# Optimization experiments

Measured on AMD Instinct MI355X. Metric: run time of the kernel, lower is better.

Reference implementation:

```python
import jax, jax.numpy as jnp
import numpy as np

B, D, H, N, K, C = 1024, 256, 512, 100000, 96, 10


def setup_inputs() -> dict:
    key = jax.random.key(0)
    ks = jax.random.split(key, 16)
    s = 0.02
    return {
        "x": jax.random.normal(ks[0], (B, D), jnp.float32),
        "candidate_x": jax.random.normal(ks[1], (N, D), jnp.float32),
        "candidate_labels": jax.random.randint(ks[2], (N,), 0, C, jnp.int32),
        "W_enc": jax.random.normal(ks[3], (D, H), jnp.float32) * s,
        "b_enc": jnp.zeros((H,), jnp.float32),
        "W_key": jax.random.normal(ks[4], (H, H), jnp.float32) * s,
        "b_key": jnp.zeros((H,), jnp.float32),
        "W_val": jax.random.normal(ks[5], (H, H), jnp.float32) * s,
        "b_val": jnp.zeros((H,), jnp.float32),
        "E_label": jax.random.normal(ks[6], (C, H), jnp.float32) * s,
        "W_t1": jax.random.normal(ks[7], (H, H), jnp.float32) * s,
        "b_t1": jnp.zeros((H,), jnp.float32),
        "W_t2": jax.random.normal(ks[8], (H, H), jnp.float32) * s,
    }


def reference(x, candidate_x, candidate_labels, W_enc, b_enc, W_key, b_key,
              W_val, b_val, E_label, W_t1, b_t1, W_t2):
    # Encode queries and candidates
    x_enc = x @ W_enc + b_enc                       # [B, H]
    cand_enc = candidate_x @ W_enc + b_enc          # [N, H]
    x_key = x_enc @ W_key + b_key                   # [B, H]
    cand_keys = cand_enc @ W_key + b_key            # [N, H]

    # Negative euclidean distance via GEMM expansion (compute-efficient cdist)
    q2 = jnp.sum(x_key * x_key, axis=-1, keepdims=True)        # [B, 1]
    c2 = jnp.sum(cand_keys * cand_keys, axis=-1)               # [N]
    d2 = q2 + c2[None, :] - 2.0 * (x_key @ cand_keys.T)        # [B, N]
    sim = -jnp.sqrt(jnp.maximum(d2, 0.0))                      # [B, N]

    # Top-k retrieval
    top_sims, top_idx = jax.lax.top_k(sim, K)                  # [B, K]

    cand_vals = cand_enc @ W_val + b_val                       # [N, H]
    label_emb = E_label[candidate_labels]                      # [N, H]

    ctx_keys = cand_keys[top_idx]                              # [B, K, H]
    ctx_labels = label_emb[top_idx]                            # [B, K, H]
    _ = cand_vals[top_idx]  # gathered values (unused by the original math)

    # Attention over retrieved context (softmax of top-k similarities)
    attn = jax.nn.softmax(top_sims, axis=1)                    # [B, K]

    # Correction MLP T (dropout is identity in eval mode)
    diff = x_key[:, None, :] - ctx_keys                        # [B, K, H]
    t_out = jax.nn.relu(diff @ W_t1 + b_t1) @ W_t2             # [B, K, H]

    ctx_vec = jnp.sum(attn[..., None] * (ctx_labels + t_out), axis=1)  # [B, H]
    return x_enc + ctx_vec
```

## Files before the change

### kernel.cpp

```cpp
#include <hip/hip_runtime.h>
#include <cfloat>
#include <cmath>

#define B_ 1024
#define D_ 256
#define H_ 512
#define N_ 100000
#define K_ 96
#define C_ 10
#define SAMP 4096
#define CAPC 4096
#define RCAP 15

typedef __attribute__((ext_vector_type(8))) short bf16x8;
typedef __attribute__((ext_vector_type(4))) float f32x4;

__device__ __forceinline__ float bf2f(ushort h) {
    union { unsigned u; float f; } v; v.u = ((unsigned)h) << 16; return v.f;
}
__device__ __forceinline__ ushort f2bf(float f) {
    union { float f; unsigned u; } v; v.f = f;
    unsigned u = v.u;
    unsigned r = (u + 0x7fffu + ((u >> 16) & 1u)) >> 16;
    return (ushort)r;
}
__device__ __forceinline__ unsigned f2key(float f) {
    unsigned u = __float_as_uint(f);
    return (u & 0x80000000u) ? ~u : (u | 0x80000000u);
}
__device__ __forceinline__ float d2_of(float acc, float q2, float c2) {
    return fmaxf(fmaf(-2.f, acc, q2 + c2), 0.f);
}

#define GLDS(g, l)                                                            \
    __builtin_amdgcn_global_load_lds(                                         \
        (const __attribute__((address_space(1))) void*)(g),                   \
        (__attribute__((address_space(3))) void*)(l), 16, 0, 0)

#define FENCE() asm volatile("" ::: "memory")

template <int RELU>
__global__ __launch_bounds__(256) void gemm_nn(const float* __restrict__ A,
                                               const float* __restrict__ Bm,
                                               const float* __restrict__ bias,
                                               float* __restrict__ Cm,
                                               int M, int N, int Kd) {
    __shared__ float sA[16][68];
    __shared__ float sB[16][64];
    const int t  = threadIdx.x;
    const int tx = t & 15, ty = t >> 4;
    const int m0 = blockIdx.y * 64;
    const int n0 = blockIdx.x * 64;
    const int lr = t >> 2;
    const int lk = (t & 3) << 2;
    const int bk = t >> 4;
    const int bn = (t & 15) << 2;

    float acc[4][4] = {};
    for (int k0 = 0; k0 < Kd; k0 += 16) {
        float4 av = make_float4(0.f, 0.f, 0.f, 0.f);
        if (m0 + lr < M)
            av = *(const float4*)(A + (size_t)(m0 + lr) * Kd + k0 + lk);
        sA[lk + 0][lr] = av.x; sA[lk + 1][lr] = av.y;
        sA[lk + 2][lr] = av.z; sA[lk + 3][lr] = av.w;
        float4 bv = *(const float4*)(Bm + (size_t)(k0 + bk) * N + n0 + bn);
        *(float4*)&sB[bk][bn] = bv;
        __syncthreads();
#pragma unroll
        for (int kk = 0; kk < 16; ++kk) {
            float4 a4 = *(const float4*)&sA[kk][ty << 2];
            float4 b4 = *(const float4*)&sB[kk][tx << 2];
            float ar[4] = {a4.x, a4.y, a4.z, a4.w};
            float br[4] = {b4.x, b4.y, b4.z, b4.w};
#pragma unroll
            for (int i = 0; i < 4; ++i)
#pragma unroll
                for (int j = 0; j < 4; ++j)
                    acc[i][j] = fmaf(ar[i], br[j], acc[i][j]);
        }
        __syncthreads();
    }
#pragma unroll
    for (int i = 0; i < 4; ++i) {
        int row = m0 + (ty << 2) + i;
        if (row < M) {
            int col = n0 + (tx << 2);
            float b0 = 0.f, b1 = 0.f, b2 = 0.f, b3 = 0.f;
            if (bias) { b0 = bias[col]; b1 = bias[col + 1]; b2 = bias[col + 2]; b3 = bias[col + 3]; }
            float4 o;
            o.x = acc[i][0] + b0; o.y = acc[i][1] + b1;
            o.z = acc[i][2] + b2; o.w = acc[i][3] + b3;
            if (RELU) {
                o.x = fmaxf(o.x, 0.f); o.y = fmaxf(o.y, 0.f);
                o.z = fmaxf(o.z, 0.f); o.w = fmaxf(o.w, 0.f);
            }
            *(float4*)(Cm + (size_t)row * N + col) = o;
        }
    }
}

template <int MODE, int SWZ>
__global__ __launch_bounds__(256) void gemm_nt(const ushort* __restrict__ A,
                                               const ushort* __restrict__ Bv,
                                               const float* __restrict__ bias,
                                               const float* __restrict__ q2v,
                                               const float* __restrict__ c2v,
                                               const float* __restrict__ thrv,
                                               float* __restrict__ candV,
                                               int* __restrict__ candI,
                                               int* __restrict__ cnt,
                                               void* __restrict__ Cout,
                                               int M, int Nlim, int K,
                                               int ldc, int nvalid, int per) {
    int m0, n0;
    if (SWZ == 0) {
        m0 = blockIdx.y * 128; n0 = blockIdx.x * 128;
    } else if (SWZ == 1) {
        int bid = blockIdx.x;
        int xcd = bid & 7, slot = bid >> 3;
        m0 = (slot & 7) * 128;
        n0 = (xcd * per + (slot >> 3)) * 128;
        if (n0 >= nvalid || m0 >= M) return;
    } else {
        int bid = blockIdx.x;
        int xcd = bid & 7, slot = bid >> 3;
        n0 = (slot & 3) * 128;
        m0 = (xcd * per + (slot >> 2)) * 128;
        if (m0 >= M) return;
    }

    __shared__ __align__(16) char smem[32768];
    const int t = threadIdx.x;
    const int lane = t & 63, w = t >> 6;
    const int wm = w & 1, wn = w >> 1;

    f32x4 acc[4][4];
#pragma unroll
    for (int i = 0; i < 4; ++i)
#pragma unroll
        for (int j = 0; j < 4; ++j)
            acc[i][j] = (f32x4){0.f, 0.f, 0.f, 0.f};

    const int la = lane & 15, lk = lane >> 4;
    const int aoff = (wm * 64 + la) * 64 + lk * 16;
    const int boff = (wn * 64 + la) * 64 + lk * 16;
    const int r_ = t >> 2, cc_ = (t & 3);

    auto stage = [&](int k0, int buf) {
#pragma unroll
        for (int q = 0; q < 2; ++q) {
            int r = r_ + q * 64;
            int ar = m0 + r; ar = (ar < M) ? ar : (M - 1);
            GLDS(A + (size_t)ar * K + k0 + cc_ * 8,
                 (char*)smem + buf * 8192 + (q * 256 + t) * 16);
            int br = n0 + r; br = (br < Nlim) ? br : (Nlim - 1);
            GLDS(Bv + (size_t)br * K + k0 + cc_ * 8,
                 (char*)smem + 16384 + buf * 8192 + (q * 256 + t) * 16);
        }
    };

    stage(0, 0);
    int cur = 0;
    for (int k0 = 0; k0 < K; k0 += 32) {
        if (k0 + 32 < K) {
            stage(k0 + 32, cur ^ 1);
            FENCE();
            asm volatile("s_waitcnt vmcnt(4)" ::: "memory");
        } else {
            FENCE();
            asm volatile("s_waitcnt vmcnt(0)" ::: "memory");
        }
        __builtin_amdgcn_s_barrier(); FENCE();

        bf16x8 af[4], bfr[4];
        const char* pA = (const char*)smem + cur * 8192 + aoff;
        const char* pB = (const char*)smem + 16384 + cur * 8192 + boff;
#pragma unroll
        for (int i = 0; i < 4; ++i)
            af[i] = *(const bf16x8*)(pA + i * 1024);
#pragma unroll
        for (int j = 0; j < 4; ++j)
            bfr[j] = *(const bf16x8*)(pB + j * 1024);
#pragma unroll
        for (int i = 0; i < 4; ++i)
#pragma unroll
            for (int j = 0; j < 4; ++j)
                acc[i][j] = __builtin_amdgcn_mfma_f32_16x16x32_bf16(
                    af[i], bfr[j], acc[i][j], 0, 0, 0);

        FENCE();
        asm volatile("s_waitcnt lgkmcnt(0)" ::: "memory");
        __builtin_amdgcn_s_barrier(); FENCE();
        cur ^= 1;
    }

    const int rl = (lane >> 4) * 4, cl = lane & 15;

    if (MODE == 5) {
        float* stV = (float*)smem;
        int*   stI = (int*)(smem + 7680);
        int*   stC = (int*)(smem + 15360);
        for (int r = t; r < 128; r += 256) stC[r] = 0;
        __syncthreads();
#pragma unroll
        for (int i = 0; i < 4; ++i) {
#pragma unroll
            for (int v = 0; v < 4; ++v) {
                int rloc = wm * 64 + i * 16 + rl + v;
                int gr = m0 + rloc;
                float q2b = q2v[gr];
                float th = thrv[gr];
#pragma unroll
                for (int j = 0; j < 4; ++j) {
                    int gc = n0 + wn * 64 + j * 16 + cl;
                    if (gc < nvalid) {
                        float d2 = d2_of(acc[i][j][v], q2b, c2v[gc]);
                        if (d2 <= th) {
                            int p = atomicAdd(&stC[rloc], 1);
                            if (p < RCAP) {
                                stV[rloc * RCAP + p] = d2;
                                stI[rloc * RCAP + p] = gc;
                            } else {
                                int gp = atomicAdd(&cnt[gr], 1);
                                if (gp < CAPC) {
                                    candV[(size_t)gr * CAPC + gp] = d2;
                                    candI[(size_t)gr * CAPC + gp] = gc;
                                }
                            }
                        }
                    }
                }
            }
        }
        __syncthreads();
        for (int r = t; r < 128; r += 256) {
            int n = stC[r]; if (n > RCAP) n = RCAP;
            if (n > 0) {
                int gr = m0 + r;
                int gb = atomicAdd(&cnt[gr], n);
                for (int q = 0; q < n; ++q) {
                    int pos = gb + q;
                    if (pos < CAPC) {
                        candV[(size_t)gr * CAPC + pos] = stV[r * RCAP + q];
                        candI[(size_t)gr * CAPC + pos] = stI[r * RCAP + q];
                    }
                }
            }
        }
        return;
    }

#pragma unroll
    for (int i = 0; i < 4; ++i) {
#pragma unroll
        for (int j = 0; j < 4; ++j) {
            int gc = n0 + wn * 64 + j * 16 + cl;
#pragma unroll
            for (int v = 0; v < 4; ++v) {
                int gr = m0 + wm * 64 + i * 16 + rl + v;
                if (gr < M && gc < nvalid) {
                    float val = acc[i][j][v];
                    if (MODE == 2) {
                        ((float*)Cout)[(size_t)gr * ldc + gc] = val;
                    } else if (MODE == 4) {
                        ((float*)Cout)[(size_t)gr * ldc + gc] = val + bias[gc];
                    } else {
                        if (MODE == 1 || MODE == 3) val += bias[gc];
                        if (MODE == 1) val = fmaxf(val, 0.f);
                        ((ushort*)Cout)[(size_t)gr * ldc + gc] = f2bf(val);
                    }
                }
            }
        }
    }
}

__global__ __launch_bounds__(256) void thr_select(const float* __restrict__ S,
                                                  int ld,
                                                  const float* __restrict__ q2v,
                                                  const float* __restrict__ c2v,
                                                  float* __restrict__ thrArr) {
    __shared__ unsigned keys[SAMP];
    __shared__ int hist[256];
    __shared__ int sel[2];
    const int b = blockIdx.x, t = threadIdx.x;
    const float q2b = q2v[b];
    for (int i = t; i < SAMP; i += 256)
        keys[i] = ~f2key(d2_of(S[(size_t)b * ld + i], q2b, c2v[i]));
    __syncthreads();
    unsigned prefix = 0, mask = 0;
    int rank = K_;
    for (int shift = 24; shift >= 0; shift -= 8) {
        hist[t & 255] = 0;
        __syncthreads();
        for (int i = t; i < SAMP; i += 256) {
            unsigned k = keys[i];
            if ((k & mask) == prefix) atomicAdd(&hist[(k >> shift) & 255], 1);
        }
        __syncthreads();
        if (t == 0) {
            int r = rank, d = 255;
            for (; d > 0; --d) { int c = hist[d]; if (r - c <= 0) break; r -= c; }
            sel[0] = d; sel[1] = (r < 1) ? 1 : r;
        }
        __syncthreads();
        prefix |= ((unsigned)sel[0]) << shift;
        rank = sel[1];
        mask |= (0xFFu << shift);
        __syncthreads();
    }
    if (t == 0) {
        unsigned key = ~prefix;
        thrArr[b] = __uint_as_float(key & 0x7FFFFFFFu);
    }
}

__global__ __launch_bounds__(256) void final_select(const float* __restrict__ candV,
                                                    const int* __restrict__ candI,
                                                    const int* __restrict__ cnt,
                                                    float* __restrict__ topV,
                                                    int* __restrict__ topI) {
    __shared__ unsigned keys[CAPC];
    __shared__ int hist[256];
    __shared__ int sel[2];
    __shared__ int poscnt, eqcnt;
    const int b = blockIdx.x, t = threadIdx.x;
    int n = cnt[b]; if (n > CAPC) n = CAPC;
    for (int i = t; i < n; i += 256)
        keys[i] = ~f2key(candV[(size_t)b * CAPC + i]);
    __syncthreads();
    unsigned prefix = 0, mask = 0;
    int rank = K_;
    for (int shift = 24; shift >= 0; shift -= 8) {
        hist[t & 255] = 0;
        __syncthreads();
        for (int i = t; i < n; i += 256) {
            unsigned k = keys[i];
            if ((k & mask) == prefix) atomicAdd(&hist[(k >> shift) & 255], 1);
        }
        __syncthreads();
        if (t == 0) {
            int r = rank, d = 255;
            for (; d > 0; --d) { int c = hist[d]; if (r - c <= 0) break; r -= c; }
            sel[0] = d; sel[1] = (r < 1) ? 1 : r;
        }
        __syncthreads();
        prefix |= ((unsigned)sel[0]) << shift;
        rank = sel[1];
        mask |= (0xFFu << shift);
        __syncthreads();
    }
    unsigned kth = prefix;
    if (t == 0) { poscnt = 0; eqcnt = 0; }
    __syncthreads();
    for (int i = t; i < n; i += 256) {
        if (keys[i] > kth) {
            int p = atomicAdd(&poscnt, 1);
            topV[b * K_ + p] = candV[(size_t)b * CAPC + i];
            topI[b * K_ + p] = candI[(size_t)b * CAPC + i];
        }
    }
    __syncthreads();
    int base = poscnt;
    for (int i = t; i < n; i += 256) {
        if (keys[i] == kth) {
            int p = atomicAdd(&eqcnt, 1);
            if (base + p < K_) {
                topV[b * K_ + base + p] = candV[(size_t)b * CAPC + i];
                topI[b * K_ + base + p] = candI[(size_t)b * CAPC + i];
            }
        }
    }
}

__global__ void init_cnt(int* cnt) {
    int i = blockIdx.x * 256 + threadIdx.x;
    if (i < B_) cnt[i] = 0;
}

__global__ void conv_f2b(const float* __restrict__ in, ushort* __restrict__ out, int n) {
    int i = (blockIdx.x * 256 + threadIdx.x) * 4;
    int stride = gridDim.x * 256 * 4;
    for (; i < n; i += stride) {
        float4 v = *(const float4*)(in + i);
        ushort4 o;
        o.x = f2bf(v.x); o.y = f2bf(v.y); o.z = f2bf(v.z); o.w = f2bf(v.w);
        *(ushort4*)(out + i) = o;
    }
}

__global__ __launch_bounds__(256) void transpose_f2b(const float* __restrict__ in,
                                                     ushort* __restrict__ out,
                                                     int R, int Cn) {
    __shared__ float tile[32][33];
    int bx = blockIdx.x * 32, by = blockIdx.y * 32;
    int tx = threadIdx.x & 31, ty = threadIdx.x >> 5;
    int x = bx + tx;
#pragma unroll
    for (int dy = 0; dy < 32; dy += 8) {
        int y = by + ty + dy;
        if (x < Cn && y < R) tile[ty + dy][tx] = in[(size_t)y * Cn + x];
    }
    __syncthreads();
    int ox = by + tx;
#pragma unroll
    for (int dy = 0; dy < 32; dy += 8) {
        int oy = bx + ty + dy;
        if (ox < R && oy < Cn) out[(size_t)oy * R + ox] = f2bf(tile[tx][ty + dy]);
    }
}

__global__ __launch_bounds__(64) void rowsq_b(const ushort* __restrict__ X,
                                              float* __restrict__ outv) {
    const int r = blockIdx.x, t = threadIdx.x;
    const ushort* p = X + (size_t)r * H_;
    ushort4 a = *(const ushort4*)(p + t * 4);
    ushort4 b = *(const ushort4*)(p + 256 + t * 4);
    float ax = bf2f(a.x), ay = bf2f(a.y), az = bf2f(a.z), aw = bf2f(a.w);
    float bx = bf2f(b.x), by = bf2f(b.y), bz = bf2f(b.z), bw = bf2f(b.w);
    float v = ax * ax + ay * ay + az * az + aw * aw +
              bx * bx + by * by + bz * bz + bw * bw;
    for (int off = 32; off > 0; off >>= 1) v += __shfl_down(v, off);
    if (t == 0) outv[r] = v;
}

__global__ __launch_bounds__(64) void q2x_k(const ushort* __restrict__ Xb,
                                            const float* __restrict__ Xf,
                                            const float* __restrict__ bc,
                                            float* __restrict__ outv) {
    const int r = blockIdx.x, t = threadIdx.x;
    const ushort* p  = Xb + (size_t)r * H_ + t * 8;
    const float*  xf = Xf + (size_t)r * H_ + t * 8;
    float nrm = 0.f, dot = 0.f;
#pragma unroll
    for (int j = 0; j < 8; ++j) {
        float v = bf2f(p[j]);
        nrm = fmaf(v, v, nrm);
        dot = fmaf(xf[j], bc[t * 8 + j], dot);
    }
    for (int off = 32; off > 0; off >>= 1) {
        nrm += __shfl_down(nrm, off);
        dot += __shfl_down(dot, off);
    }
    if (t == 0) outv[r] = nrm - 2.f * dot;
}

__global__ void bcomb_k(const float* __restrict__ b_enc,
                        const float* __restrict__ W_key,
                        const float* __restrict__ b_key,
                        float* __restrict__ b_comb) {
    int h = blockIdx.x * 256 + threadIdx.x;
    if (h >= H_) return;
    float acc = b_key[h];
    for (int m = 0; m < H_; ++m)
        acc = fmaf(b_enc[m], W_key[(size_t)m * H_ + h], acc);
    b_comb[h] = acc;
}

__global__ __launch_bounds__(128) void softmax_k(const float* __restrict__ topVal,
                                                 float* __restrict__ attn) {
    __shared__ float red[128];
    const int b = blockIdx.x, t = threadIdx.x;
    float v = (t < K_) ? -sqrtf(topVal[b * K_ + t]) : -FLT_MAX;
    red[t] = v; __syncthreads();
    for (int s = 64; s > 0; s >>= 1) {
        if (t < s) red[t] = fmaxf(red[t], red[t + s]);
        __syncthreads();
    }
    float m = red[0]; __syncthreads();
    float e = (t < K_) ? expf(v - m) : 0.f;
    red[t] = e; __syncthreads();
    for (int s = 64; s > 0; s >>= 1) {
        if (t < s) red[t] += red[t + s];
        __syncthreads();
    }
    float ssum = red[0];
    if (t < K_) attn[b * K_ + t] = e / ssum;
}

__global__ __launch_bounds__(256) void wsum_q(const float* __restrict__ attn,
                                              const int* __restrict__ topI,
                                              const float* __restrict__ P,
                                              const ushort* __restrict__ Q,
                                              ushort* __restrict__ hw) {
    __shared__ float aw[K_];
    __shared__ int ai[K_];
    const int b = blockIdx.x, t = threadIdx.x;
    if (t < K_) { aw[t] = attn[b * K_ + t]; ai[t] = topI[b * K_ + t]; }
    __syncthreads();
    const float p0 = P[(size_t)b * H_ + 2 * t];
    const float p1 = P[(size_t)b * H_ + 2 * t + 1];
    float a0 = 0.f, a1 = 0.f;
    for (int k = 0; k < K_; ++k) {
        float w = aw[k];
        ushort2 q = *(const ushort2*)(Q + (size_t)ai[k] * H_ + 2 * t);
        a0 = fmaf(w, fmaxf(p0 - bf2f(q.x), 0.f), a0);
        a1 = fmaf(w, fmaxf(p1 - bf2f(q.y), 0.f), a1);
    }
    ushort2 o; o.x = f2bf(a0); o.y = f2bf(a1);
    *(ushort2*)(hw + (size_t)b * H_ + 2 * t) = o;
}

__global__ __launch_bounds__(128) void gather_diff_b(const float* __restrict__ XK,
                                                     const ushort* __restrict__ CK,
                                                     const int* __restrict__ topI,
                                                     ushort* __restrict__ diff,
                                                     int b0) {
    const int r = blockIdx.x;
    const int b = b0 + r / K_;
    const int idx = topI[b * K_ + (r % K_)];
    const int t = threadIdx.x;
    float4 xv = *(const float4*)(XK + (size_t)b * H_ + t * 4);
    ushort4 cv = *(const ushort4*)(CK + (size_t)idx * H_ + t * 4);
    ushort4 o;
    o.x = f2bf(xv.x - bf2f(cv.x));
    o.y = f2bf(xv.y - bf2f(cv.y));
    o.z = f2bf(xv.z - bf2f(cv.z));
    o.w = f2bf(xv.w - bf2f(cv.w));
    *(ushort4*)(diff + (size_t)r * H_ + t * 4) = o;
}

__global__ __launch_bounds__(256) void wsum_h(const float* __restrict__ attn,
                                              const ushort* __restrict__ h,
                                              ushort* __restrict__ hw, int b0) {
    const int bl = blockIdx.x;
    const int b = b0 + bl;
    const int t = threadIdx.x;
    float a0 = 0.f, a1 = 0.f;
    const float* ap = attn + b * K_;
    for (int k = 0; k < K_; ++k) {
        float w = ap[k];
        const ushort* hr = h + (size_t)(bl * K_ + k) * H_;
        a0 = fmaf(w, bf2f(hr[t]), a0);
        a1 = fmaf(w, bf2f(hr[t + 256]), a1);
    }
    hw[(size_t)b * H_ + t]       = f2bf(a0);
    hw[(size_t)b * H_ + t + 256] = f2bf(a1);
}

__global__ __launch_bounds__(256) void final_out(const float* __restrict__ attn,
                                                 const int* __restrict__ topI,
                                                 const int* __restrict__ labels,
                                                 const float* __restrict__ E,
                                                 const float* __restrict__ tsum,
                                                 const float* __restrict__ xe,
                                                 float* __restrict__ out) {
    const int b = blockIdx.x, t = threadIdx.x;
    float a0 = 0.f, a1 = 0.f;
    for (int k = 0; k < K_; ++k) {
        float w = attn[b * K_ + k];
        int idx = topI[b * K_ + k];
        int lab = labels[idx];
        const float* el = E + (size_t)lab * H_;
        a0 = fmaf(w, el[t], a0);
        a1 = fmaf(w, el[t + 256], a1);
    }
    out[(size_t)b * H_ + t] =
        xe[(size_t)b * H_ + t] + a0 + tsum[(size_t)b * H_ + t];
    out[(size_t)b * H_ + t + 256] =
        xe[(size_t)b * H_ + t + 256] + a1 + tsum[(size_t)b * H_ + t + 256];
}

extern "C" void kernel_launch(void* const* d_in, const int* in_sizes, int n_in,
                              void* d_out, int out_size, void* d_ws, size_t ws_size,
                              hipStream_t stream) {
    const float* x      = (const float*)d_in[0];
    const float* cx     = (const float*)d_in[1];
    const int*   labels = (const int*)d_in[2];
    const float* W_enc  = (const float*)d_in[3];
    const float* b_enc  = (const float*)d_in[4];
    const float* W_key  = (const float*)d_in[5];
    const float* b_key  = (const float*)d_in[6];
    const float* E_label = (const float*)d_in[9];
    const float* W_t1   = (const float*)d_in[10];
    const float* b_t1   = (const float*)d_in[11];
    const float* W_t2   = (const float*)d_in[12];
    float* out = (float*)d_out;

    char* base = (char*)d_ws;
    size_t off = 0;
    auto take = [&](size_t n) -> char* {
        char* p = base + off;
        off = (off + n + 255) & ~(size_t)255;
        return p;
    };
    float*  Wc    = (float*)take((size_t)D_ * H_ * 4);
    float*  bc    = (float*)take((size_t)H_ * 4);
    ushort* WcT   = (ushort*)take((size_t)H_ * D_ * 2);
    ushort* Wcb   = (ushort*)take((size_t)D_ * H_ * 2);
    ushort* Wt1T  = (ushort*)take((size_t)H_ * H_ * 2);
    ushort* Wt2T  = (ushort*)take((size_t)H_ * H_ * 2);
    float*  xe    = (float*)take((size_t)B_ * H_ * 4);
    float*  xk    = (float*)take((size_t)B_ * H_ * 4);
    ushort* xkb   = (ushort*)take((size_t)B_ * H_ * 2);
    ushort* xprojb= (ushort*)take((size_t)B_ * D_ * 2);
    float*  q2x   = (float*)take((size_t)B_ * 4);
    ushort* ckb   = (ushort*)take((size_t)N_ * H_ * 2);
    float*  c2    = (float*)take((size_t)N_ * 4);
    float*  topV  = (float*)take((size_t)B_ * K_ * 4);
    int*    topI  = (int*)take((size_t)B_ * K_ * 4);
    float*  thr   = (float*)take((size_t)B_ * 4);
    float*  attn  = (float*)take((size_t)B_ * K_ * 4);
    int*    cnt   = (int*)take((size_t)B_ * 4);
    float*  candV = (float*)take((size_t)B_ * CAPC * 4);
    int*    candI = (int*)take((size_t)B_ * CAPC * 4);
    ushort* hwAll = (ushort*)take((size_t)B_ * H_ * 2);
    float*  tsum  = (float*)take((size_t)B_ * H_ * 4);
    float*  Pbuf  = (float*)take((size_t)B_ * H_ * 4);
    char*   big   = base + off;
    size_t rem = (ws_size > off) ? (ws_size - off) : 0;

    ushort* cxb = (ushort*)big;
    float* simSmall = (float*)candV;

    {
        dim3 g(H_ / 64, D_ / 64);
        gemm_nn<0><<<g, 256, 0, stream>>>(W_enc, W_key, nullptr, Wc, D_, H_, H_);
        bcomb_k<<<(H_ + 255) / 256, 256, 0, stream>>>(b_enc, W_key, b_key, bc);
        dim3 gt1((H_ + 31) / 32, (D_ + 31) / 32);
        transpose_f2b<<<gt1, 256, 0, stream>>>(Wc, WcT, D_, H_);
        conv_f2b<<<128, 256, 0, stream>>>(Wc, Wcb, D_ * H_);
        dim3 gt2((H_ + 31) / 32, (H_ + 31) / 32);
        transpose_f2b<<<gt2, 256, 0, stream>>>(W_t1, Wt1T, H_, H_);
        transpose_f2b<<<gt2, 256, 0, stream>>>(W_t2, Wt2T, H_, H_);
    }
    {
        dim3 gx(H_ / 64, B_ / 64);
        gemm_nn<0><<<gx, 256, 0, stream>>>(x, W_enc, b_enc, xe, B_, H_, D_);
        gemm_nn<0><<<gx, 256, 0, stream>>>(x, Wc, bc, xk, B_, H_, D_);
        conv_f2b<<<1024, 256, 0, stream>>>(xk, xkb, B_ * H_);
        conv_f2b<<<2048, 256, 0, stream>>>(cx, cxb, N_ * D_);
        dim3 gp(D_ / 128, B_ / 128);
        gemm_nt<0, 0><<<gp, 256, 0, stream>>>(
            xkb, Wcb, nullptr, nullptr, nullptr, nullptr, nullptr, nullptr,
            nullptr, xprojb, B_, D_, H_, D_, D_, 0);
        q2x_k<<<B_, 64, 0, stream>>>(xkb, xk, bc, q2x);
        dim3 gq(H_ / 128, B_ / 128);
        gemm_nt<4, 0><<<gq, 256, 0, stream>>>(
            xkb, Wt1T, b_t1, nullptr, nullptr, nullptr, nullptr, nullptr,
            nullptr, Pbuf, B_, H_, H_, H_, H_, 0);
    }
    {
        int mt = (N_ + 127) / 128;
        int mper = (mt + 7) / 8;
        gemm_nt<3, 2><<<8 * mper * 4, 256, 0, stream>>>(
            cxb, WcT, bc, nullptr, nullptr, nullptr, nullptr, nullptr, nullptr,
            ckb, N_, H_, D_, H_, H_, mper);
    }
    rowsq_b<<<N_, 64, 0, stream>>>(ckb, c2);

    {
        int nper = (SAMP / 128 + 7) / 8;
        gemm_nt<2, 1><<<64 * nper, 256, 0, stream>>>(
            xprojb, cxb, nullptr, nullptr, nullptr, nullptr, nullptr, nullptr,
            nullptr, simSmall, B_, N_, D_, SAMP, SAMP, nper);
        thr_select<<<B_, 256, 0, stream>>>(simSmall, SAMP, q2x, c2, thr);
    }
    init_cnt<<<(B_ + 255) / 256, 256, 0, stream>>>(cnt);
    {
        int NT = (N_ + 127) / 128;
        int nper = (NT + 7) / 8;
        gemm_nt<5, 1><<<64 * nper, 256, 0, stream>>>(
            xprojb, cxb, nullptr, q2x, c2, thr, candV, candI, cnt,
            nullptr, B_, N_, D_, 0, N_, nper);
    }
    final_select<<<B_, 256, 0, stream>>>(candV, candI, cnt, topV, topI);
    softmax_k<<<B_, 128, 0, stream>>>(topV, attn);

    if (rem >= (size_t)N_ * H_ * 2) {
        ushort* Qb = (ushort*)big;
        int mt = (N_ + 127) / 128;
        int mper = (mt + 7) / 8;
        gemm_nt<0, 2><<<8 * mper * 4, 256, 0, stream>>>(
            ckb, Wt1T, nullptr, nullptr, nullptr, nullptr, nullptr, nullptr,
            nullptr, Qb, N_, H_, H_, H_, H_, mper);
        wsum_q<<<B_, 256, 0, stream>>>(attn, topI, Pbuf, Qb, hwAll);
    } else {
        long long bcq = (long long)(rem / ((size_t)K_ * H_ * 2 * 2));
        if (bcq > B_) bcq = B_;
        if (bcq < 1) bcq = 1;
        int Bc = (int)bcq;
        ushort* diffB = (ushort*)big;
        ushort* hB = (ushort*)(big + (size_t)Bc * K_ * H_ * 2);
        for (int b0 = 0; b0 < B_; b0 += Bc) {
            int bcn = min(Bc, B_ - b0);
            int Mrows = bcn * K_;
            gather_diff_b<<<Mrows, 128, 0, stream>>>(xk, ckb, topI, diffB, b0);
            int mt4 = (Mrows + 127) / 128;
            int mper4 = (mt4 + 7) / 8;
            gemm_nt<1, 2><<<8 * mper4 * 4, 256, 0, stream>>>(
                diffB, Wt1T, b_t1, nullptr, nullptr, nullptr, nullptr, nullptr,
                nullptr, hB, Mrows, H_, H_, H_, H_, mper4);
            wsum_h<<<bcn, 256, 0, stream>>>(attn, hB, hwAll, b0);
        }
    }
    {
        dim3 g(H_ / 128, B_ / 128);
        gemm_nt<2, 0><<<g, 256, 0, stream>>>(
            hwAll, Wt2T, nullptr, nullptr, nullptr, nullptr, nullptr, nullptr,
            nullptr, tsum, B_, H_, H_, H_, H_, 0);
    }
    final_out<<<B_, 256, 0, stream>>>(attn, topI, labels, E_label, tsum, xe, out);
}
```

Measured before the change: 854.3 us.

## Fold candidate key GEMM into norm reduction and precompose W_t1 projection

The materialised candidate key matrix (N×H bf16) is no longer written. A new GEMM epilogue mode computes the squared row norms directly via shuffle reduction and atomics into a zeroed buffer. The per-candidate W_t1 projection is now computed straight from the candidate inputs with a precomposed weight (Wc·W_t1) and bias, replacing the chained H×H GEMM over stored keys. The gather-diff fallback path is removed. This cuts one large GEMM's K dimension and a large write and read of candidate keys, at the cost of atomics and always needing workspace for Qb. Precomposing the weights changes the rounding path.

```diff
diff --git a/kernel.cpp b/kernel.cpp
--- a/kernel.cpp
+++ b/kernel.cpp
@@ -196,6 +196,30 @@
 
     const int rl = (lane >> 4) * 4, cl = lane & 15;
 
+    if (MODE == 7) {
+#pragma unroll
+        for (int i = 0; i < 4; ++i) {
+#pragma unroll
+            for (int v = 0; v < 4; ++v) {
+                int gr = m0 + wm * 64 + i * 16 + rl + v;
+                float s = 0.f;
+#pragma unroll
+                for (int j = 0; j < 4; ++j) {
+                    int gc = n0 + wn * 64 + j * 16 + cl;
+                    float val = acc[i][j][v] + bias[gc];
+                    float vb = bf2f(f2bf(val));
+                    s = fmaf(vb, vb, s);
+                }
+                s += __shfl_xor(s, 1);
+                s += __shfl_xor(s, 2);
+                s += __shfl_xor(s, 4);
+                s += __shfl_xor(s, 8);
+                if (cl == 0 && gr < M) atomicAdd(&candV[gr], s);
+            }
+        }
+        return;
+    }
+
     if (MODE == 5) {
         float* stV = (float*)smem;
         int*   stI = (int*)(smem + 7680);
@@ -265,8 +289,7 @@
                     } else if (MODE == 4) {
                         ((float*)Cout)[(size_t)gr * ldc + gc] = val + bias[gc];
                     } else {
-                        if (MODE == 1 || MODE == 3) val += bias[gc];
-                        if (MODE == 1) val = fmaxf(val, 0.f);
+                        if (MODE == 3) val += bias[gc];
                         ((ushort*)Cout)[(size_t)gr * ldc + gc] = f2bf(val);
                     }
                 }
@@ -378,6 +401,12 @@
     if (i < B_) cnt[i] = 0;
 }
 
+__global__ void init_f32(float* p, int n) {
+    int i = blockIdx.x * 256 + threadIdx.x;
+    int stride = gridDim.x * 256;
+    for (; i < n; i += stride) p[i] = 0.f;
+}
+
 __global__ void conv_f2b(const float* __restrict__ in, ushort* __restrict__ out, int n) {
     int i = (blockIdx.x * 256 + threadIdx.x) * 4;
     int stride = gridDim.x * 256 * 4;
@@ -408,20 +437,6 @@
         int oy = bx + ty + dy;
         if (ox < R && oy < Cn) out[(size_t)oy * R + ox] = f2bf(tile[tx][ty + dy]);
     }
-}
-
-__global__ __launch_bounds__(64) void rowsq_b(const ushort* __restrict__ X,
-                                              float* __restrict__ outv) {
-    const int r = blockIdx.x, t = threadIdx.x;
-    const ushort* p = X + (size_t)r * H_;
-    ushort4 a = *(const ushort4*)(p + t * 4);
-    ushort4 b = *(const ushort4*)(p + 256 + t * 4);
-    float ax = bf2f(a.x), ay = bf2f(a.y), az = bf2f(a.z), aw = bf2f(a.w);
-    float bx = bf2f(b.x), by = bf2f(b.y), bz = bf2f(b.z), bw = bf2f(b.w);
-    float v = ax * ax + ay * ay + az * az + aw * aw +
-              bx * bx + by * by + bz * bz + bw * bw;
-    for (int off = 32; off > 0; off >>= 1) v += __shfl_down(v, off);
-    if (t == 0) outv[r] = v;
 }
 
 __global__ __launch_bounds__(64) void q2x_k(const ushort* __restrict__ Xb,
@@ -455,6 +470,17 @@
     for (int m = 0; m < H_; ++m)
         acc = fmaf(b_enc[m], W_key[(size_t)m * H_ + h], acc);
     b_comb[h] = acc;
+}
+
+__global__ void bq_k(const float* __restrict__ bc,
+                     const float* __restrict__ W1,
+                     float* __restrict__ bq) {
+    int h = blockIdx.x * 256 + threadIdx.x;
+    if (h >= H_) return;
+    float acc = 0.f;
+    for (int m = 0; m < H_; ++m)
+        acc = fmaf(bc[m], W1[(size_t)m * H_ + h], acc);
+    bq[h] = acc;
 }
 
 __global__ __launch_bounds__(128) void softmax_k(const float* __restrict__ topVal,
@@ -501,43 +527,6 @@
     *(ushort2*)(hw + (size_t)b * H_ + 2 * t) = o;
 }
 
-__global__ __launch_bounds__(128) void gather_diff_b(const float* __restrict__ XK,
-                                                     const ushort* __restrict__ CK,
-                                                     const int* __restrict__ topI,
-                                                     ushort* __restrict__ diff,
-                                                     int b0) {
-    const int r = blockIdx.x;
-    const int b = b0 + r / K_;
-    const int idx = topI[b * K_ + (r % K_)];
-    const int t = threadIdx.x;
-    float4 xv = *(const float4*)(XK + (size_t)b * H_ + t * 4);
-    ushort4 cv = *(const ushort4*)(CK + (size_t)idx * H_ + t * 4);
-    ushort4 o;
-    o.x = f2bf(xv.x - bf2f(cv.x));
-    o.y = f2bf(xv.y - bf2f(cv.y));
-    o.z = f2bf(xv.z - bf2f(cv.z));
-    o.w = f2bf(xv.w - bf2f(cv.w));
-    *(ushort4*)(diff + (size_t)r * H_ + t * 4) = o;
-}
-
-__global__ __launch_bounds__(256) void wsum_h(const float* __restrict__ attn,
-                                              const ushort* __restrict__ h,
-                                              ushort* __restrict__ hw, int b0) {
-    const int bl = blockIdx.x;
-    const int b = b0 + bl;
-    const int t = threadIdx.x;
-    float a0 = 0.f, a1 = 0.f;
-    const float* ap = attn + b * K_;
-    for (int k = 0; k < K_; ++k) {
-        float w = ap[k];
-        const ushort* hr = h + (size_t)(bl * K_ + k) * H_;
-        a0 = fmaf(w, bf2f(hr[t]), a0);
-        a1 = fmaf(w, bf2f(hr[t + 256]), a1);
-    }
-    hw[(size_t)b * H_ + t]       = f2bf(a0);
-    hw[(size_t)b * H_ + t + 256] = f2bf(a1);
-}
-
 __global__ __launch_bounds__(256) void final_out(const float* __restrict__ attn,
                                                  const int* __restrict__ topI,
                                                  const int* __restrict__ labels,
@@ -588,6 +577,9 @@
     float*  bc    = (float*)take((size_t)H_ * 4);
     ushort* WcT   = (ushort*)take((size_t)H_ * D_ * 2);
     ushort* Wcb   = (ushort*)take((size_t)D_ * H_ * 2);
+    float*  Wq    = (float*)take((size_t)D_ * H_ * 4);
+    ushort* WqT   = (ushort*)take((size_t)H_ * D_ * 2);
+    float*  bq    = (float*)take((size_t)H_ * 4);
     ushort* Wt1T  = (ushort*)take((size_t)H_ * H_ * 2);
     ushort* Wt2T  = (ushort*)take((size_t)H_ * H_ * 2);
     float*  xe    = (float*)take((size_t)B_ * H_ * 4);
@@ -595,7 +587,6 @@
     ushort* xkb   = (ushort*)take((size_t)B_ * H_ * 2);
     ushort* xprojb= (ushort*)take((size_t)B_ * D_ * 2);
     float*  q2x   = (float*)take((size_t)B_ * 4);
-    ushort* ckb   = (ushort*)take((size_t)N_ * H_ * 2);
     float*  c2    = (float*)take((size_t)N_ * 4);
     float*  topV  = (float*)take((size_t)B_ * K_ * 4);
     int*    topI  = (int*)take((size_t)B_ * K_ * 4);
@@ -607,8 +598,8 @@
     ushort* hwAll = (ushort*)take((size_t)B_ * H_ * 2);
     float*  tsum  = (float*)take((size_t)B_ * H_ * 4);
     float*  Pbuf  = (float*)take((size_t)B_ * H_ * 4);
+    ushort* Qb    = (ushort*)take((size_t)N_ * H_ * 2);
     char*   big   = base + off;
-    size_t rem = (ws_size > off) ? (ws_size - off) : 0;
 
     ushort* cxb = (ushort*)big;
     float* simSmall = (float*)candV;
@@ -617,8 +608,11 @@
         dim3 g(H_ / 64, D_ / 64);
         gemm_nn<0><<<g, 256, 0, stream>>>(W_enc, W_key, nullptr, Wc, D_, H_, H_);
         bcomb_k<<<(H_ + 255) / 256, 256, 0, stream>>>(b_enc, W_key, b_key, bc);
+        gemm_nn<0><<<g, 256, 0, stream>>>(Wc, W_t1, nullptr, Wq, D_, H_, H_);
+        bq_k<<<(H_ + 255) / 256, 256, 0, stream>>>(bc, W_t1, bq);
         dim3 gt1((H_ + 31) / 32, (D_ + 31) / 32);
         transpose_f2b<<<gt1, 256, 0, stream>>>(Wc, WcT, D_, H_);
+        transpose_f2b<<<gt1, 256, 0, stream>>>(Wq, WqT, D_, H_);
         conv_f2b<<<128, 256, 0, stream>>>(Wc, Wcb, D_ * H_);
         dim3 gt2((H_ + 31) / 32, (H_ + 31) / 32);
         transpose_f2b<<<gt2, 256, 0, stream>>>(W_t1, Wt1T, H_, H_);
@@ -640,14 +634,14 @@
             xkb, Wt1T, b_t1, nullptr, nullptr, nullptr, nullptr, nullptr,
             nullptr, Pbuf, B_, H_, H_, H_, H_, 0);
     }
+    init_f32<<<128, 256, 0, stream>>>(c2, N_);
     {
         int mt = (N_ + 127) / 128;
         int mper = (mt + 7) / 8;
-        gemm_nt<3, 2><<<8 * mper * 4, 256, 0, stream>>>(
-            cxb, WcT, bc, nullptr, nullptr, nullptr, nullptr, nullptr, nullptr,
-            ckb, N_, H_, D_, H_, H_, mper);
-    }
-    rowsq_b<<<N_, 64, 0, stream>>>(ckb, c2);
+        gemm_nt<7, 2><<<8 * mper * 4, 256, 0, stream>>>(
+            cxb, WcT, bc, nullptr, nullptr, nullptr, c2, nullptr, nullptr,
+            nullptr, N_, H_, D_, H_, H_, mper);
+    }
 
     {
         int nper = (SAMP / 128 + 7) / 8;
@@ -664,36 +658,17 @@
             xprojb, cxb, nullptr, q2x, c2, thr, candV, candI, cnt,
             nullptr, B_, N_, D_, 0, N_, nper);
     }
+    {
+        int mt = (N_ + 127) / 128;
+        int mper = (mt + 7) / 8;
+        gemm_nt<3, 2><<<8 * mper * 4, 256, 0, stream>>>(
+            cxb, WqT, bq, nullptr, nullptr, nullptr, nullptr, nullptr,
+            nullptr, Qb, N_, H_, D_, H_, H_, mper);
+    }
     final_select<<<B_, 256, 0, stream>>>(candV, candI, cnt, topV, topI);
     softmax_k<<<B_, 128, 0, stream>>>(topV, attn);
 
-    if (rem >= (size_t)N_ * H_ * 2) {
-        ushort* Qb = (ushort*)big;
-        int mt = (N_ + 127) / 128;
-        int mper = (mt + 7) / 8;
-        gemm_nt<0, 2><<<8 * mper * 4, 256, 0, stream>>>(
-            ckb, Wt1T, nullptr, nullptr, nullptr, nullptr, nullptr, nullptr,
-            nullptr, Qb, N_, H_, H_, H_, H_, mper);
-        wsum_q<<<B_, 256, 0, stream>>>(attn, topI, Pbuf, Qb, hwAll);
-    } else {
-        long long bcq = (long long)(rem / ((size_t)K_ * H_ * 2 * 2));
-        if (bcq > B_) bcq = B_;
-        if (bcq < 1) bcq = 1;
-        int Bc = (int)bcq;
-        ushort* diffB = (ushort*)big;
-        ushort* hB = (ushort*)(big + (size_t)Bc * K_ * H_ * 2);
-        for (int b0 = 0; b0 < B_; b0 += Bc) {
-            int bcn = min(Bc, B_ - b0);
-            int Mrows = bcn * K_;
-            gather_diff_b<<<Mrows, 128, 0, stream>>>(xk, ckb, topI, diffB, b0);
-            int mt4 = (Mrows + 127) / 128;
-            int mper4 = (mt4 + 7) / 8;
-            gemm_nt<1, 2><<<8 * mper4 * 4, 256, 0, stream>>>(
-                diffB, Wt1T, b_t1, nullptr, nullptr, nullptr, nullptr, nullptr,
-                nullptr, hB, Mrows, H_, H_, H_, H_, mper4);
-            wsum_h<<<bcn, 256, 0, stream>>>(attn, hB, hwAll, b0);
-        }
-    }
+    wsum_q<<<B_, 256, 0, stream>>>(attn, topI, Pbuf, Qb, hwAll);
     {
         dim3 g(H_ / 128, B_ / 128);
         gemm_nt<2, 0><<<g, 256, 0, stream>>>(
```

New measurement: 835.8 us. 1.02x faster.
